# Optimization experiments

Hardware: AMD Instinct MI355X
Metric: run time of the kernel (lower is better)

## Reference

```python
import jax, jax.numpy as jnp
import numpy as np

NGROUP = 16
CIN = 8    # per-group input channels
COUT = 8   # per-group output channels
K = 1
HIDDEN = True  # output group g may see input groups <= g
B, H, W = 4, 512, 512


def group_mask(ngroup, cout, cin, k, hidden):
    go = jnp.arange(ngroup * cout) // cout           # out-group id per out channel
    gi = jnp.arange(ngroup * cin) // cin             # in-group id per in channel
    if hidden:
        m = (gi[None, :] <= go[:, None])             # include current group
    else:
        m = (gi[None, :] < go[:, None])
    return m.astype(jnp.float32)[:, :, None, None]   # [Cout*g, Cin*g, 1, 1]


def setup_inputs() -> dict:
    key = jax.random.key(0)
    k1, k2, k3 = jax.random.split(key, 3)
    x = jax.random.normal(k1, (B, NGROUP * CIN, H, W), dtype=jnp.float32)
    weight = jax.random.normal(k2, (NGROUP * COUT, NGROUP * CIN, K, K), dtype=jnp.float32) * 0.05
    bias = jax.random.normal(k3, (NGROUP * COUT,), dtype=jnp.float32) * 0.01
    return {"x": x, "weight": weight, "bias": bias}


def reference(x, weight, bias):
    mask = group_mask(NGROUP, COUT, CIN, K, HIDDEN)
    wt = weight * mask                               # block-lower-triangular weight
    out = jax.lax.conv_general_dilated(
        x, wt,
        window_strides=(1, 1), padding='VALID',
        dimension_numbers=('NCHW', 'OIHW', 'NCHW'))
    return out + bias[None, :, None, None]
```

## Files before the change

### kernel.cpp

```cpp
#include <hip/hip_runtime.h>


#define HW        (512 * 512)
#define NPIX_TILE 64
#define NTILES    (4 * HW / NPIX_TILE)

typedef __attribute__((ext_vector_type(8))) short bf16x8;
typedef __attribute__((ext_vector_type(4))) float f32x4;

__device__ inline unsigned short f2bf_rne(float f) {
    unsigned u = __float_as_uint(f);
    u += 0x7FFFu + ((u >> 16) & 1u);
    return (unsigned short)(u >> 16);
}

__global__ __launch_bounds__(256, 2)
void cgc_mfma_kernel(const float* __restrict__ x, const float* __restrict__ w,
                     const float* __restrict__ bias, float* __restrict__ out,
                     int ntiles) {
    const int tid  = threadIdx.x;
    const int lane = tid & 63;
    const int wv   = tid >> 6;
    const int quad = lane >> 4;
    const int l16  = lane & 15;

    bf16x8 afrag[8][4];
    #pragma unroll
    for (int t = 0; t < 8; ++t) {
        const int co   = 16 * t + l16;
        const int klim = (co & ~7) + 8;
        #pragma unroll
        for (int kk = 0; kk <= t / 2; ++kk) {
            const int k0 = 32 * kk + quad * 8;
            const float* wp = w + co * 128 + k0;
            bf16x8 f;
            #pragma unroll
            for (int j = 0; j < 8; ++j) {
                float v = (k0 < klim) ? wp[j] : 0.0f;
                f[j] = (short)f2bf_rne(v);
            }
            afrag[t][kk] = f;
        }
    }

    f32x4 biasr[8];
    #pragma unroll
    for (int t = 0; t < 8; ++t)
        #pragma unroll
        for (int r = 0; r < 4; ++r)
            biasr[t][r] = bias[16 * t + quad * 4 + r];

    for (int tile = blockIdx.x; tile < ntiles; tile += gridDim.x) {
        const int b = tile >> 12;
        const int p = ((tile & 4095) << 6) + (wv << 4) + l16;
        const size_t base = ((size_t)b << 25) + (size_t)p;

        const float* xp = x + base + ((size_t)(quad * 8) << 18);
        float fv[4][8];
        #pragma unroll
        for (int kk = 0; kk < 4; ++kk)
            #pragma unroll
            for (int j = 0; j < 8; ++j)
                fv[kk][j] = xp[(size_t)(kk * 32 + j) << 18];

        bf16x8 bfrag[4];
        #pragma unroll
        for (int kk = 0; kk < 4; ++kk) {
            bf16x8 f;
            #pragma unroll
            for (int j = 0; j < 8; ++j) f[j] = (short)f2bf_rne(fv[kk][j]);
            bfrag[kk] = f;
        }

        f32x4 acc[8];
        #pragma unroll
        for (int t = 0; t < 8; ++t) acc[t] = biasr[t];
        #pragma unroll
        for (int kk = 0; kk < 4; ++kk)
            #pragma unroll
            for (int t = 2 * kk; t < 8; ++t)
                acc[t] = __builtin_amdgcn_mfma_f32_16x16x32_bf16(
                    afrag[t][kk], bfrag[kk], acc[t], 0, 0, 0);

        float* op = out + base + ((size_t)(quad * 4) << 18);
        #pragma unroll
        for (int t = 0; t < 8; ++t)
            #pragma unroll
            for (int r = 0; r < 4; ++r)
                op[(size_t)(16 * t + r) << 18] = acc[t][r];
    }
}

extern "C" void kernel_launch(void* const* d_in, const int* in_sizes, int n_in,
                              void* d_out, int out_size, void* d_ws, size_t ws_size,
                              hipStream_t stream) {
    const float* x    = (const float*)d_in[0];
    const float* w    = (const float*)d_in[1];
    const float* bias = (const float*)d_in[2];
    float* out        = (float*)d_out;

    dim3 grid(2048), block(256);
    hipLaunchKernelGGL(cgc_mfma_kernel, grid, block, 0, stream,
                       x, w, bias, out, NTILES);
}
```

Measured before the change: 925.7 us.

## Stage input tile through swizzled LDS with vectorized loads and stores

New measurement: 903.1 us. -2.4%, faster.

```diff
diff --git a/kernel.cpp b/kernel.cpp
--- a/kernel.cpp
+++ b/kernel.cpp
@@ -1,30 +1,31 @@
 #include <hip/hip_runtime.h>
 
 
-#define HW        (512 * 512)
-#define NPIX_TILE 64
-#define NTILES    (4 * HW / NPIX_TILE)
+#define HW     (512 * 512)
+#define TPX    256
+#define NTILES (4 * HW / TPX)
 
 typedef __attribute__((ext_vector_type(8))) short bf16x8;
 typedef __attribute__((ext_vector_type(4))) float f32x4;
 
-__device__ inline unsigned short f2bf_rne(float f) {
+__device__ inline unsigned rne32(float f) {
     unsigned u = __float_as_uint(f);
-    u += 0x7FFFu + ((u >> 16) & 1u);
-    return (unsigned short)(u >> 16);
+    return u + 0x7FFFu + ((u >> 16) & 1u);
 }
 
 __global__ __launch_bounds__(256, 2)
 void cgc_mfma_kernel(const float* __restrict__ x, const float* __restrict__ w,
                      const float* __restrict__ bias, float* __restrict__ out,
                      int ntiles) {
+    __shared__ unsigned char lds[TPX * 128 * 2];
+
     const int tid  = threadIdx.x;
     const int lane = tid & 63;
     const int wv   = tid >> 6;
     const int quad = lane >> 4;
     const int l16  = lane & 15;
 
-    bf16x8 afrag[8][4];
+    bf16x8 wfrag[8][4];
     #pragma unroll
     for (int t = 0; t < 8; ++t) {
         const int co   = 16 * t + l16;
@@ -37,57 +38,76 @@
             #pragma unroll
             for (int j = 0; j < 8; ++j) {
                 float v = (k0 < klim) ? wp[j] : 0.0f;
-                f[j] = (short)f2bf_rne(v);
+                f[j] = (short)(rne32(v) >> 16);
             }
-            afrag[t][kk] = f;
+            wfrag[t][kk] = f;
         }
     }
 
-    f32x4 biasr[8];
+    float biasv[8];
     #pragma unroll
-    for (int t = 0; t < 8; ++t)
-        #pragma unroll
-        for (int r = 0; r < 4; ++r)
-            biasr[t][r] = bias[16 * t + quad * 4 + r];
+    for (int t = 0; t < 8; ++t) biasv[t] = bias[16 * t + l16];
 
     for (int tile = blockIdx.x; tile < ntiles; tile += gridDim.x) {
-        const int b = tile >> 12;
-        const int p = ((tile & 4095) << 6) + (wv << 4) + l16;
-        const size_t base = ((size_t)b << 25) + (size_t)p;
+        const int b      = tile >> 10;
+        const int pxbase = (tile & 1023) << 8;
+        const size_t xoff = ((size_t)(b * 128) << 18) + (size_t)pxbase;
 
-        const float* xp = x + base + ((size_t)(quad * 8) << 18);
-        float fv[4][8];
+        __syncthreads();
+
+        {
+            const float* pbase = x + xoff + 4 * lane;
+            #pragma unroll 4
+            for (int i = 0; i < 16; ++i) {
+                const int ci0 = 8 * i + 2 * wv;
+                const float* pa = pbase + ((size_t)ci0 << 18);
+                f32x4 A = *(const f32x4*)pa;
+                f32x4 B = *(const f32x4*)(pa + (1 << 18));
+                #pragma unroll
+                for (int d = 0; d < 4; ++d) {
+                    unsigned pk = (rne32(B[d]) & 0xFFFF0000u) | (rne32(A[d]) >> 16);
+                    const int px   = 4 * lane + d;
+                    const int byte = ((((i * TPX + px) << 4) + 4 * wv)
+                                     ^ (((px >> 2) & 7) << 4));
+                    *(unsigned*)(lds + byte) = pk;
+                }
+            }
+        }
+        __syncthreads();
+
         #pragma unroll
-        for (int kk = 0; kk < 4; ++kk)
+        for (int s = 0; s < 4; ++s) {
+            const int p0 = 64 * wv + 16 * s;
+            const int px = p0 + l16;
+
+            bf16x8 xf[4];
             #pragma unroll
-            for (int j = 0; j < 8; ++j)
-                fv[kk][j] = xp[(size_t)(kk * 32 + j) << 18];
+            for (int kk = 0; kk < 4; ++kk) {
+                const int byte = ((((4 * kk + quad) * TPX + px) << 4)
+                                 ^ (((px >> 2) & 7) << 4));
+                xf[kk] = *(const bf16x8*)(lds + byte);
+            }
 
-        bf16x8 bfrag[4];
-        #pragma unroll
-        for (int kk = 0; kk < 4; ++kk) {
-            bf16x8 f;
+            f32x4 acc[8];
             #pragma unroll
-            for (int j = 0; j < 8; ++j) f[j] = (short)f2bf_rne(fv[kk][j]);
-            bfrag[kk] = f;
+            for (int t = 0; t < 8; ++t) {
+                f32x4 a; a[0] = a[1] = a[2] = a[3] = biasv[t];
+                acc[t] = a;
+            }
+            #pragma unroll
+            for (int kk = 0; kk < 4; ++kk)
+                #pragma unroll
+                for (int t = 2 * kk; t < 8; ++t)
+                    acc[t] = __builtin_amdgcn_mfma_f32_16x16x32_bf16(
+                        xf[kk], wfrag[t][kk], acc[t], 0, 0, 0);
+
+            #pragma unroll
+            for (int t = 0; t < 8; ++t) {
+                float* op = out + xoff + ((size_t)(16 * t + l16) << 18)
+                            + p0 + 4 * quad;
+                *(f32x4*)op = acc[t];
+            }
         }
-
-        f32x4 acc[8];
-        #pragma unroll
-        for (int t = 0; t < 8; ++t) acc[t] = biasr[t];
-        #pragma unroll
-        for (int kk = 0; kk < 4; ++kk)
-            #pragma unroll
-            for (int t = 2 * kk; t < 8; ++t)
-                acc[t] = __builtin_amdgcn_mfma_f32_16x16x32_bf16(
-                    afrag[t][kk], bfrag[kk], acc[t], 0, 0, 0);
-
-        float* op = out + base + ((size_t)(quad * 4) << 18);
-        #pragma unroll
-        for (int t = 0; t < 8; ++t)
-            #pragma unroll
-            for (int r = 0; r < 4; ++r)
-                op[(size_t)(16 * t + r) << 18] = acc[t][r];
     }
 }
 
@@ -99,7 +119,7 @@
     const float* bias = (const float*)d_in[2];
     float* out        = (float*)d_out;
 
-    dim3 grid(2048), block(256);
+    dim3 grid(512), block(256);
     hipLaunchKernelGGL(cgc_mfma_kernel, grid, block, 0, stream,
                        x, w, bias, out, NTILES);
 }
```
